# Kernel optimization log

Measured on AMD Instinct MI355X. Metric: run time of the kernel, lower is better.

## Reference

```python
import jax, jax.numpy as jnp
import numpy as np

B, N, D, P, V = 8, 256, 300, 128, 50001  # batch, seq len, emb dim, proj dim, vocab(+unk)


def setup_inputs() -> dict:
    key = jax.random.key(0)
    ks = jax.random.split(key, 10)
    s = 1.0 / np.sqrt(D)
    sp = 1.0 / np.sqrt(P)
    emb = jax.random.normal(ks[0], (V, D), jnp.float32)
    emb = emb.at[-1].set(0.0)  # unk row zeroed, matches add_unk
    return {
        "sentence": jax.random.randint(ks[1], (B, N), 0, V),
        "emb": emb,
        "Wl": jax.random.uniform(ks[2], (P, D), jnp.float32, -s, s),
        "bl": jnp.zeros((P,), jnp.float32),
        "Wr": jax.random.uniform(ks[3], (P, D), jnp.float32, -s, s),
        "Wo": jax.random.uniform(ks[4], (1, P), jnp.float32, -sp, sp),
        "bo": jnp.zeros((1,), jnp.float32),
        "Ws1": jax.random.uniform(ks[5], (P, D), jnp.float32, -s, s),
        "bs1": jnp.zeros((P,), jnp.float32),
        "Ws2": jax.random.uniform(ks[6], (1, P), jnp.float32, -sp, sp),
        "bs2": jnp.zeros((1,), jnp.float32),
        "We1": jax.random.uniform(ks[7], (P, D), jnp.float32, -s, s),
        "be1": jnp.zeros((P,), jnp.float32),
        "We2": jax.random.uniform(ks[8], (1, P), jnp.float32, -sp, sp),
        "be2": jnp.zeros((1,), jnp.float32),
    }


def reference(sentence, emb, Wl, bl, Wr, Wo, bo, Ws1, bs1, Ws2, bs2, We1, be1, We2, be2):
    x = emb[sentence]                                   # [B,N,D] embedding lookup
    start = jax.nn.relu(x @ Ws1.T + bs1) @ Ws2.T + bs2  # [B,N,1]
    end = jax.nn.relu(x @ We1.T + be1) @ We2.T + be2    # [B,N,1]
    left = x @ Wl.T + bl                                # [B,N,P]
    right = x @ Wr.T                                    # [B,N,P]
    # proj[b,i,j,p] = left[b,j,p] + right[b,i,p]  (unsqueeze(1) + unsqueeze(2))
    proj = left[:, None, :, :] + right[:, :, None, :]   # [B,N,N,P]
    bigram = jax.nn.relu(proj) @ Wo.T + bo              # [B,N,N,1]
    return (bigram, start, end)
```

## Files before the change

kernel.cpp:

```cpp
#include <hip/hip_runtime.h>

#define NB 8
#define NN 256
#define DD 300
#define PP 128
#define NC 512
#define OFF_S (NB * NN * NN)
#define OFF_E (NB * NN * NN + NB * NN)

typedef unsigned short u16;
typedef unsigned int   u32;

__device__ __forceinline__ float bf2f(u16 u) {
    union { u32 i; float f; } v;
    v.i = ((u32)u) << 16;
    return v.f;
}
__device__ __forceinline__ u16 f2bf(float f) {
    union { float f; u32 i; } v;
    v.f = f;
    u32 lsb = (v.i >> 16) & 1u;
    v.i += 0x7fffu + lsb;
    return (u16)(v.i >> 16);
}

template<bool BF>
__device__ __forceinline__ float4 ld4(const void* base, int idx) {
    if (BF) {
        ushort4 e = *(const ushort4*)((const u16*)base + idx);
        return make_float4(bf2f(e.x), bf2f(e.y), bf2f(e.z), bf2f(e.w));
    } else {
        return *(const float4*)((const float*)base + idx);
    }
}
template<bool BF>
__device__ __forceinline__ float ld1(const void* base, int idx) {
    return BF ? bf2f(((const u16*)base)[idx]) : ((const float*)base)[idx];
}
template<bool BF>
__device__ __forceinline__ void st1(void* base, int idx, float v) {
    if (BF) ((u16*)base)[idx] = f2bf(v);
    else    ((float*)base)[idx] = v;
}
template<bool BF>
__device__ __forceinline__ void st4(void* base, int idx, float4 v) {
    if (BF) {
        ushort4 o = make_ushort4(f2bf(v.x), f2bf(v.y), f2bf(v.z), f2bf(v.w));
        *(ushort4*)((u16*)base + idx) = o;
    } else {
        *(float4*)((float*)base + idx) = v;
    }
}
__device__ __forceinline__ float4 rfma4(float4 l, float r, float w, float4 a) {
    a.x = fmaf(fmaxf(l.x + r, 0.f), w, a.x);
    a.y = fmaf(fmaxf(l.y + r, 0.f), w, a.y);
    a.z = fmaf(fmaxf(l.z + r, 0.f), w, a.z);
    a.w = fmaf(fmaxf(l.w + r, 0.f), w, a.w);
    return a;
}

extern "C" __global__ void detect_kernel(const u32* __restrict__ embU,
                                         int* __restrict__ flag) {
    int lane = threadIdx.x;
    int cnt = 0;
    for (int i = lane; i < 256; i += 64) {
        u32 w = embU[i];
        union { u32 u; float f; } v;
        v.u = (w & 0xFFFFu) << 16;
        float a = fabsf(v.f);
        if (a == 0.f || (a >= 0.00390625f && a <= 256.f)) cnt++;
    }
    #pragma unroll
    for (int off = 32; off; off >>= 1) cnt += __shfl_down(cnt, off, 64);
    if (lane == 0) *flag = (cnt >= 128) ? 1 : 0;
}

template<bool BF>
__device__ __forceinline__ void prep_body(
    const void* __restrict__ Wl, const void* __restrict__ Wr,
    const void* __restrict__ Ws1, const void* __restrict__ We1,
    const int* __restrict__ sent, const void* __restrict__ emb,
    float* __restrict__ WTf, float* __restrict__ xf, float (*tile)[301])
{
    const int tid = threadIdx.x;

    if (blockIdx.x < 16) {
        const int c0 = blockIdx.x * 32;
        for (int e = tid; e < 32 * 75; e += 256) {
            int r = e / 75;
            int q = e - r * 75;
            int c = c0 + r;
            const void* src = (c < 128) ? Wl : (c < 256) ? Wr
                            : (c < 384) ? Ws1 : We1;
            float4 f = ld4<BF>(src, (c & 127) * DD + 4 * q);
            tile[r][4 * q + 0] = f.x;
            tile[r][4 * q + 1] = f.y;
            tile[r][4 * q + 2] = f.z;
            tile[r][4 * q + 3] = f.w;
        }
        __syncthreads();
        for (int e = tid; e < 300 * 32; e += 256) {
            int k = e >> 5;
            int c = e & 31;
            WTf[(size_t)k * NC + c0 + c] = tile[c][k];
        }
    } else {
        const int t0g = (blockIdx.x - 16) * 64;
        for (int e = tid; e < 64 * DD; e += 256) {
            int t = e / DD;
            int k = e - t * DD;
            int idx = sent[t0g + t];
            xf[(size_t)(t0g + t) * DD + k] = ld1<BF>(emb, idx * DD + k);
        }
    }
}

extern "C" __global__ void __launch_bounds__(256)
prep_kernel(const void* __restrict__ Wl, const void* __restrict__ Wr,
            const void* __restrict__ Ws1, const void* __restrict__ We1,
            const int* __restrict__ sent, const void* __restrict__ emb,
            float* __restrict__ WTf, float* __restrict__ xf,
            const int* __restrict__ flag)
{
    __shared__ float tile[32][301];
    if (*flag) prep_body<true >(Wl, Wr, Ws1, We1, sent, emb, WTf, xf, tile);
    else       prep_body<false>(Wl, Wr, Ws1, We1, sent, emb, WTf, xf, tile);
}

template<bool BF>
__device__ __forceinline__ void tok_body(
    const float* __restrict__ WTf, const float* __restrict__ xf,
    const void* __restrict__ bl,
    const void* __restrict__ bs1, const void* __restrict__ Ws2,
    const void* __restrict__ bs2,
    const void* __restrict__ be1, const void* __restrict__ We2,
    const void* __restrict__ be2,
    float* __restrict__ leftT, float* __restrict__ rightW,
    void* __restrict__ out)
{
    const int tid   = threadIdx.x;
    const int t0    = blockIdx.x * 8;
    const int half  = tid >> 7;
    const int l127  = tid & 127;
    const int col4  = l127 * 4;
    const int tbase = t0 + 4 * half;

    const float* x0 = xf + (size_t)(tbase + 0) * DD;
    const float* x1 = xf + (size_t)(tbase + 1) * DD;
    const float* x2 = xf + (size_t)(tbase + 2) * DD;
    const float* x3 = xf + (size_t)(tbase + 3) * DD;
    const float* wrow = WTf + col4;

    float a0[4] = {0,0,0,0}, a1[4] = {0,0,0,0};
    float a2[4] = {0,0,0,0}, a3[4] = {0,0,0,0};

    #pragma unroll 4
    for (int k = 0; k < DD; ++k) {
        float4 w = *(const float4*)(wrow + (size_t)k * NC);
        float s0 = x0[k], s1 = x1[k], s2 = x2[k], s3 = x3[k];
        a0[0] = fmaf(w.x, s0, a0[0]); a0[1] = fmaf(w.y, s0, a0[1]);
        a0[2] = fmaf(w.z, s0, a0[2]); a0[3] = fmaf(w.w, s0, a0[3]);
        a1[0] = fmaf(w.x, s1, a1[0]); a1[1] = fmaf(w.y, s1, a1[1]);
        a1[2] = fmaf(w.z, s1, a1[2]); a1[3] = fmaf(w.w, s1, a1[3]);
        a2[0] = fmaf(w.x, s2, a2[0]); a2[1] = fmaf(w.y, s2, a2[1]);
        a2[2] = fmaf(w.z, s2, a2[2]); a2[3] = fmaf(w.w, s2, a2[3]);
        a3[0] = fmaf(w.x, s3, a3[0]); a3[1] = fmaf(w.y, s3, a3[1]);
        a3[2] = fmaf(w.z, s3, a3[2]); a3[3] = fmaf(w.w, s3, a3[3]);
    }

    const int m = l127 >> 5;
    const int p = col4 & 127;

    if (m == 0) {
        float b[4];
        #pragma unroll
        for (int r = 0; r < 4; ++r) b[r] = ld1<BF>(bl, p + r);
        const int bb = tbase >> 8;
        #pragma unroll
        for (int tt = 0; tt < 4; ++tt) {
            const int jj = (tbase + tt) & 255;
            float* acc = (tt == 0) ? a0 : (tt == 1) ? a1 : (tt == 2) ? a2 : a3;
            #pragma unroll
            for (int r = 0; r < 4; ++r)
                leftT[((size_t)bb * PP + p + r) * NN + jj] = acc[r] + b[r];
        }
    } else if (m == 1) {
        #pragma unroll
        for (int tt = 0; tt < 4; ++tt) {
            float* acc = (tt == 0) ? a0 : (tt == 1) ? a1 : (tt == 2) ? a2 : a3;
            *(float4*)(rightW + (size_t)(tbase + tt) * PP + p) =
                make_float4(acc[0], acc[1], acc[2], acc[3]);
        }
    } else {
        const void* h1 = (m == 2) ? bs1 : be1;
        const void* h2 = (m == 2) ? Ws2 : We2;
        const void* h3 = (m == 2) ? bs2 : be2;
        float b1[4], w2[4];
        #pragma unroll
        for (int r = 0; r < 4; ++r) {
            b1[r] = ld1<BF>(h1, p + r);
            w2[r] = ld1<BF>(h2, p + r);
        }
        float v[4];
        #pragma unroll
        for (int tt = 0; tt < 4; ++tt) {
            float* acc = (tt == 0) ? a0 : (tt == 1) ? a1 : (tt == 2) ? a2 : a3;
            float s = 0.f;
            #pragma unroll
            for (int r = 0; r < 4; ++r)
                s += fmaxf(acc[r] + b1[r], 0.f) * w2[r];
            v[tt] = s;
        }
        #pragma unroll
        for (int off = 16; off; off >>= 1) {
            #pragma unroll
            for (int tt = 0; tt < 4; ++tt)
                v[tt] += __shfl_down(v[tt], off, 32);
        }
        if ((l127 & 31) == 0) {
            float b2 = ld1<BF>(h3, 0);
            int base = (m == 2) ? OFF_S : OFF_E;
            #pragma unroll
            for (int tt = 0; tt < 4; ++tt)
                st1<BF>(out, base + tbase + tt, v[tt] + b2);
        }
    }
}

extern "C" __global__ void __launch_bounds__(256)
tok_kernel(const float* __restrict__ WTf, const float* __restrict__ xf,
           const void* __restrict__ bl,
           const void* __restrict__ bs1, const void* __restrict__ Ws2,
           const void* __restrict__ bs2,
           const void* __restrict__ be1, const void* __restrict__ We2,
           const void* __restrict__ be2,
           float* __restrict__ leftT, float* __restrict__ rightW,
           void* __restrict__ out, const int* __restrict__ flag)
{
    if (*flag) {
        tok_body<true >(WTf, xf, bl, bs1, Ws2, bs2, be1, We2, be2,
                        leftT, rightW, out);
    } else {
        tok_body<false>(WTf, xf, bl, bs1, Ws2, bs2, be1, We2, be2,
                        leftT, rightW, out);
    }
}

template<bool BF>
__device__ __forceinline__ void big_body(
    const float* __restrict__ leftT, const float* __restrict__ rightW,
    const void* __restrict__ Wo, const void* __restrict__ bo,
    void* __restrict__ outB,
    float (*sR)[128], float* sWo, float4 (*red4)[64][4])
{
    const int tid = threadIdx.x;
    const int b   = blockIdx.x >> 6;
    const int i0  = (blockIdx.x & 63) << 2;

    if (tid < 128) sWo[tid] = ld1<BF>(Wo, tid);
    for (int c = tid; c < 512; c += 256) {
        int i = c >> 7, pp = c & 127;
        sR[i][pp] = rightW[((size_t)(b * NN + i0 + i)) * PP + pp];
    }
    __syncthreads();

    const int w    = tid >> 6;
    const int lane = tid & 63;
    const int j4   = lane << 2;
    const float* lp = leftT + (size_t)b * PP * NN + j4;

    float4 A0 = {0.f, 0.f, 0.f, 0.f}, A1 = A0, A2 = A0, A3 = A0;
    const int pbase = w * 32;
    #pragma unroll
    for (int g = 0; g < 8; ++g) {
        const int p = pbase + g * 4;
        float4 wo = *(const float4*)&sWo[p];
        float4 r0 = *(const float4*)&sR[0][p];
        float4 r1 = *(const float4*)&sR[1][p];
        float4 r2 = *(const float4*)&sR[2][p];
        float4 r3 = *(const float4*)&sR[3][p];
        const float* lpp = lp + (size_t)p * NN;
        float4 l0 = *(const float4*)(lpp);
        float4 l1 = *(const float4*)(lpp + NN);
        float4 l2 = *(const float4*)(lpp + 2 * NN);
        float4 l3 = *(const float4*)(lpp + 3 * NN);
        A0 = rfma4(l0, r0.x, wo.x, A0);
        A1 = rfma4(l0, r1.x, wo.x, A1);
        A2 = rfma4(l0, r2.x, wo.x, A2);
        A3 = rfma4(l0, r3.x, wo.x, A3);
        A0 = rfma4(l1, r0.y, wo.y, A0);
        A1 = rfma4(l1, r1.y, wo.y, A1);
        A2 = rfma4(l1, r2.y, wo.y, A2);
        A3 = rfma4(l1, r3.y, wo.y, A3);
        A0 = rfma4(l2, r0.z, wo.z, A0);
        A1 = rfma4(l2, r1.z, wo.z, A1);
        A2 = rfma4(l2, r2.z, wo.z, A2);
        A3 = rfma4(l2, r3.z, wo.z, A3);
        A0 = rfma4(l3, r0.w, wo.w, A0);
        A1 = rfma4(l3, r1.w, wo.w, A1);
        A2 = rfma4(l3, r2.w, wo.w, A2);
        A3 = rfma4(l3, r3.w, wo.w, A3);
    }

    red4[w][lane][0] = A0;
    red4[w][lane][1] = A1;
    red4[w][lane][2] = A2;
    red4[w][lane][3] = A3;
    __syncthreads();

    if (tid < 64) {
        float bov = ld1<BF>(bo, 0);
        #pragma unroll
        for (int i = 0; i < 4; ++i) {
            float4 s0 = red4[0][tid][i];
            float4 s1 = red4[1][tid][i];
            float4 s2 = red4[2][tid][i];
            float4 s3 = red4[3][tid][i];
            float4 s;
            s.x = s0.x + s1.x + s2.x + s3.x + bov;
            s.y = s0.y + s1.y + s2.y + s3.y + bov;
            s.z = s0.z + s1.z + s2.z + s3.z + bov;
            s.w = s0.w + s1.w + s2.w + s3.w + bov;
            st4<BF>(outB, (int)(((size_t)(b * NN + i0 + i)) * NN) + tid * 4, s);
        }
    }
}

extern "C" __global__ void __launch_bounds__(256)
big_kernel(const float* __restrict__ leftT, const float* __restrict__ rightW,
           const void* __restrict__ Wo, const void* __restrict__ bo,
           void* __restrict__ outB, const int* __restrict__ flag)
{
    __shared__ float sR[4][128];
    __shared__ float sWo[128];
    __shared__ float4 red4[4][64][4];
    if (*flag) big_body<true >(leftT, rightW, Wo, bo, outB, sR, sWo, red4);
    else       big_body<false>(leftT, rightW, Wo, bo, outB, sR, sWo, red4);
}

extern "C" void kernel_launch(void* const* d_in, const int* in_sizes, int n_in,
                              void* d_out, int out_size, void* d_ws, size_t ws_size,
                              hipStream_t stream) {
    const int*  sent = (const int*)d_in[0];
    const void* emb  = d_in[1];
    const void* Wl   = d_in[2];
    const void* bl   = d_in[3];
    const void* Wr   = d_in[4];
    const void* Wo   = d_in[5];
    const void* bo   = d_in[6];
    const void* Ws1  = d_in[7];
    const void* bs1  = d_in[8];
    const void* Ws2  = d_in[9];
    const void* bs2  = d_in[10];
    const void* We1  = d_in[11];
    const void* be1  = d_in[12];
    const void* We2  = d_in[13];
    const void* be2  = d_in[14];

    int*   flag   = (int*)d_ws;
    float* leftT  = (float*)((char*)d_ws + 1024);
    float* rightW = leftT + (size_t)NB * PP * NN;
    float* WTf    = rightW + (size_t)NB * NN * PP;
    float* xf     = WTf + (size_t)DD * NC;

    hipLaunchKernelGGL(detect_kernel, dim3(1), dim3(64), 0, stream,
                       (const u32*)emb, flag);
    hipLaunchKernelGGL(prep_kernel, dim3(48), dim3(256), 0, stream,
                       Wl, Wr, Ws1, We1, sent, emb, WTf, xf, flag);
    hipLaunchKernelGGL(tok_kernel, dim3(256), dim3(256), 0, stream,
                       WTf, xf, bl, bs1, Ws2, bs2, be1, We2, be2,
                       leftT, rightW, d_out, flag);
    hipLaunchKernelGGL(big_kernel, dim3(512), dim3(256), 0, stream,
                       leftT, rightW, Wo, bo, d_out, flag);
}
```

Measured before the change: 182.3 us.

## Fuse embedding gather into token kernel via shared-memory transposed tile

Result: faster. 163.0 us (-10.6%).

```diff
diff --git a/kernel.cpp b/kernel.cpp
--- a/kernel.cpp
+++ b/kernel.cpp
@@ -79,93 +79,86 @@
 __device__ __forceinline__ void prep_body(
     const void* __restrict__ Wl, const void* __restrict__ Wr,
     const void* __restrict__ Ws1, const void* __restrict__ We1,
-    const int* __restrict__ sent, const void* __restrict__ emb,
-    float* __restrict__ WTf, float* __restrict__ xf, float (*tile)[301])
+    float* __restrict__ WTf, float (*tile)[301])
 {
     const int tid = threadIdx.x;
-
-    if (blockIdx.x < 16) {
-        const int c0 = blockIdx.x * 32;
-        for (int e = tid; e < 32 * 75; e += 256) {
-            int r = e / 75;
-            int q = e - r * 75;
-            int c = c0 + r;
-            const void* src = (c < 128) ? Wl : (c < 256) ? Wr
-                            : (c < 384) ? Ws1 : We1;
-            float4 f = ld4<BF>(src, (c & 127) * DD + 4 * q);
-            tile[r][4 * q + 0] = f.x;
-            tile[r][4 * q + 1] = f.y;
-            tile[r][4 * q + 2] = f.z;
-            tile[r][4 * q + 3] = f.w;
-        }
-        __syncthreads();
-        for (int e = tid; e < 300 * 32; e += 256) {
-            int k = e >> 5;
-            int c = e & 31;
-            WTf[(size_t)k * NC + c0 + c] = tile[c][k];
-        }
-    } else {
-        const int t0g = (blockIdx.x - 16) * 64;
-        for (int e = tid; e < 64 * DD; e += 256) {
-            int t = e / DD;
-            int k = e - t * DD;
-            int idx = sent[t0g + t];
-            xf[(size_t)(t0g + t) * DD + k] = ld1<BF>(emb, idx * DD + k);
-        }
+    const int c0  = blockIdx.x * 32;
+
+    for (int e = tid; e < 32 * 75; e += 256) {
+        int r = e / 75;
+        int q = e - r * 75;
+        int c = c0 + r;
+        const void* src = (c < 128) ? Wl : (c < 256) ? Wr
+                        : (c < 384) ? Ws1 : We1;
+        float4 f = ld4<BF>(src, (c & 127) * DD + 4 * q);
+        tile[r][4 * q + 0] = f.x;
+        tile[r][4 * q + 1] = f.y;
+        tile[r][4 * q + 2] = f.z;
+        tile[r][4 * q + 3] = f.w;
+    }
+    __syncthreads();
+    for (int e = tid; e < 300 * 32; e += 256) {
+        int k = e >> 5;
+        int c = e & 31;
+        WTf[(size_t)k * NC + c0 + c] = tile[c][k];
     }
 }
 
 extern "C" __global__ void __launch_bounds__(256)
 prep_kernel(const void* __restrict__ Wl, const void* __restrict__ Wr,
             const void* __restrict__ Ws1, const void* __restrict__ We1,
-            const int* __restrict__ sent, const void* __restrict__ emb,
-            float* __restrict__ WTf, float* __restrict__ xf,
-            const int* __restrict__ flag)
+            float* __restrict__ WTf, const int* __restrict__ flag)
 {
     __shared__ float tile[32][301];
-    if (*flag) prep_body<true >(Wl, Wr, Ws1, We1, sent, emb, WTf, xf, tile);
-    else       prep_body<false>(Wl, Wr, Ws1, We1, sent, emb, WTf, xf, tile);
+    if (*flag) prep_body<true >(Wl, Wr, Ws1, We1, WTf, tile);
+    else       prep_body<false>(Wl, Wr, Ws1, We1, WTf, tile);
 }
 
 template<bool BF>
 __device__ __forceinline__ void tok_body(
-    const float* __restrict__ WTf, const float* __restrict__ xf,
+    const int* __restrict__ sent, const void* __restrict__ emb,
+    const float* __restrict__ WTf,
     const void* __restrict__ bl,
     const void* __restrict__ bs1, const void* __restrict__ Ws2,
     const void* __restrict__ bs2,
     const void* __restrict__ be1, const void* __restrict__ We2,
     const void* __restrict__ be2,
     float* __restrict__ leftT, float* __restrict__ rightW,
-    void* __restrict__ out)
-{
-    const int tid   = threadIdx.x;
-    const int t0    = blockIdx.x * 8;
-    const int half  = tid >> 7;
-    const int l127  = tid & 127;
-    const int col4  = l127 * 4;
+    void* __restrict__ out, float (*sxT)[8], int* sids)
+{
+    const int tid = threadIdx.x;
+    const int t0  = blockIdx.x * 8;
+
+    if (tid < 8) sids[tid] = sent[t0 + tid];
+    __syncthreads();
+
+    for (int e = tid; e < DD * 8; e += 256) {
+        int k = e >> 3, t = e & 7;
+        sxT[k][t] = ld1<BF>(emb, sids[t] * DD + k);
+    }
+    __syncthreads();
+
+    const int half = tid >> 7;
+    const int l127 = tid & 127;
+    const int col4 = l127 * 4;
     const int tbase = t0 + 4 * half;
-
-    const float* x0 = xf + (size_t)(tbase + 0) * DD;
-    const float* x1 = xf + (size_t)(tbase + 1) * DD;
-    const float* x2 = xf + (size_t)(tbase + 2) * DD;
-    const float* x3 = xf + (size_t)(tbase + 3) * DD;
-    const float* wrow = WTf + col4;
 
     float a0[4] = {0,0,0,0}, a1[4] = {0,0,0,0};
     float a2[4] = {0,0,0,0}, a3[4] = {0,0,0,0};
 
+    const float* wrow = WTf + col4;
     #pragma unroll 4
     for (int k = 0; k < DD; ++k) {
         float4 w = *(const float4*)(wrow + (size_t)k * NC);
-        float s0 = x0[k], s1 = x1[k], s2 = x2[k], s3 = x3[k];
-        a0[0] = fmaf(w.x, s0, a0[0]); a0[1] = fmaf(w.y, s0, a0[1]);
-        a0[2] = fmaf(w.z, s0, a0[2]); a0[3] = fmaf(w.w, s0, a0[3]);
-        a1[0] = fmaf(w.x, s1, a1[0]); a1[1] = fmaf(w.y, s1, a1[1]);
-        a1[2] = fmaf(w.z, s1, a1[2]); a1[3] = fmaf(w.w, s1, a1[3]);
-        a2[0] = fmaf(w.x, s2, a2[0]); a2[1] = fmaf(w.y, s2, a2[1]);
-        a2[2] = fmaf(w.z, s2, a2[2]); a2[3] = fmaf(w.w, s2, a2[3]);
-        a3[0] = fmaf(w.x, s3, a3[0]); a3[1] = fmaf(w.y, s3, a3[1]);
-        a3[2] = fmaf(w.z, s3, a3[2]); a3[3] = fmaf(w.w, s3, a3[3]);
+        float4 x = *(const float4*)&sxT[k][4 * half];
+        a0[0] = fmaf(w.x, x.x, a0[0]); a0[1] = fmaf(w.y, x.x, a0[1]);
+        a0[2] = fmaf(w.z, x.x, a0[2]); a0[3] = fmaf(w.w, x.x, a0[3]);
+        a1[0] = fmaf(w.x, x.y, a1[0]); a1[1] = fmaf(w.y, x.y, a1[1]);
+        a1[2] = fmaf(w.z, x.y, a1[2]); a1[3] = fmaf(w.w, x.y, a1[3]);
+        a2[0] = fmaf(w.x, x.z, a2[0]); a2[1] = fmaf(w.y, x.z, a2[1]);
+        a2[2] = fmaf(w.z, x.z, a2[2]); a2[3] = fmaf(w.w, x.z, a2[3]);
+        a3[0] = fmaf(w.x, x.w, a3[0]); a3[1] = fmaf(w.y, x.w, a3[1]);
+        a3[2] = fmaf(w.z, x.w, a3[2]); a3[3] = fmaf(w.w, x.w, a3[3]);
     }
 
     const int m = l127 >> 5;
@@ -228,7 +221,8 @@
 }
 
 extern "C" __global__ void __launch_bounds__(256)
-tok_kernel(const float* __restrict__ WTf, const float* __restrict__ xf,
+tok_kernel(const int* __restrict__ sent, const void* __restrict__ emb,
+           const float* __restrict__ WTf,
            const void* __restrict__ bl,
            const void* __restrict__ bs1, const void* __restrict__ Ws2,
            const void* __restrict__ bs2,
@@ -237,12 +231,14 @@
            float* __restrict__ leftT, float* __restrict__ rightW,
            void* __restrict__ out, const int* __restrict__ flag)
 {
+    __shared__ __align__(16) float sxT[DD][8];
+    __shared__ int sids[8];
     if (*flag) {
-        tok_body<true >(WTf, xf, bl, bs1, Ws2, bs2, be1, We2, be2,
-                        leftT, rightW, out);
+        tok_body<true >(sent, emb, WTf, bl, bs1, Ws2, bs2, be1, We2, be2,
+                        leftT, rightW, out, sxT, sids);
     } else {
-        tok_body<false>(WTf, xf, bl, bs1, Ws2, bs2, be1, We2, be2,
-                        leftT, rightW, out);
+        tok_body<false>(sent, emb, WTf, bl, bs1, Ws2, bs2, be1, We2, be2,
+                        leftT, rightW, out, sxT, sids);
     }
 }
 
@@ -361,14 +357,13 @@
     float* leftT  = (float*)((char*)d_ws + 1024);
     float* rightW = leftT + (size_t)NB * PP * NN;
     float* WTf    = rightW + (size_t)NB * NN * PP;
-    float* xf     = WTf + (size_t)DD * NC;
 
     hipLaunchKernelGGL(detect_kernel, dim3(1), dim3(64), 0, stream,
                        (const u32*)emb, flag);
-    hipLaunchKernelGGL(prep_kernel, dim3(48), dim3(256), 0, stream,
-                       Wl, Wr, Ws1, We1, sent, emb, WTf, xf, flag);
+    hipLaunchKernelGGL(prep_kernel, dim3(16), dim3(256), 0, stream,
+                       Wl, Wr, Ws1, We1, WTf, flag);
     hipLaunchKernelGGL(tok_kernel, dim3(256), dim3(256), 0, stream,
-                       WTf, xf, bl, bs1, Ws2, bs2, be1, We2, be2,
+                       sent, emb, WTf, bl, bs1, Ws2, bs2, be1, We2, be2,
                        leftT, rightW, d_out, flag);
     hipLaunchKernelGGL(big_kernel, dim3(512), dim3(256), 0, stream,
                        leftT, rightW, Wo, bo, d_out, flag);
```
